# Optimization experiments

Hardware: AMD Instinct MI355X
Metric: run time of the kernel (lower is better)

## Reference

```python
import jax, jax.numpy as jnp
import numpy as np

VQ_NUM = 3
EMB_NUM = 1024
COMMITMENT_WEIGHT = 1.0
# cumprod of [1, emb_num, emb_num] -> per-stage index bases
CUMPROD = [1, EMB_NUM, EMB_NUM * EMB_NUM]


def setup_inputs() -> dict:
    key = jax.random.key(0)
    k0, k1, k2, k3 = jax.random.split(key, 4)
    z = jax.random.normal(k0, (8, 4096, 512), dtype=jnp.float32)
    # linear_in: nn.Linear(in_ch=512, emb_ch=256, bias=False) -> weight [emb_ch, in_ch]
    W_in = jax.random.normal(k1, (VQ_NUM, 256, 512), dtype=jnp.float32) * 0.02
    # linear_out: nn.Linear(emb_ch=256, in_ch=512, bias=False) -> weight [in_ch, emb_ch]
    W_out = jax.random.normal(k2, (VQ_NUM, 512, 256), dtype=jnp.float32) * 0.02
    # one codebook per stage (share_residual_codebooks=False)
    codebooks = jax.random.normal(k3, (VQ_NUM, EMB_NUM, 256), dtype=jnp.float32) * 0.02
    return {"z": z, "W_in": W_in, "W_out": W_out, "codebooks": codebooks}


def reference(z, W_in, W_out, codebooks):
    sg = jax.lax.stop_gradient
    z_q = jnp.zeros_like(z)
    r = z
    loss = jnp.float32(0.0)
    index_sum = jnp.zeros(z.shape[:2], dtype=jnp.int64 if jax.config.jax_enable_x64 else jnp.int32)
    for i in range(VQ_NUM):
        # linear_in
        zi = jnp.einsum('bnc,ec->bne', r, W_in[i])  # [B,N,emb_ch]
        v = codebooks[i]  # [S, emb_ch]
        # squared L2 distance: ||z||^2 + ||v||^2 - 2 z.v
        dist = (jnp.sum(zi * zi, axis=-1, keepdims=True)
                + jnp.sum(v * v, axis=-1)
                - 2.0 * jnp.einsum('bne,se->bns', zi, v))  # [B,N,S]
        idx = jnp.argmin(dist, axis=-1)  # [B,N] int
        zq = v[idx]  # codebook lookup, [B,N,emb_ch]
        loss = loss + (COMMITMENT_WEIGHT * jnp.mean((sg(zq) - zi) ** 2)
                       + jnp.mean((zq - sg(zi)) ** 2))
        # straight-through estimator
        zq_ste = zi + sg(zq - zi)
        # linear_out
        r_q = jnp.einsum('bne,ce->bnc', zq_ste, W_out[i])  # [B,N,in_ch]
        index_sum = index_sum + idx.astype(index_sum.dtype) * CUMPROD[i]
        z_q = z_q + r_q
        r = z - sg(z_q)
    loss = loss / VQ_NUM + jnp.mean((z_q - z) ** 2)
    return z_q, index_sum, loss
```

## Files before the change

### kernel.cpp

```cpp
#include <hip/hip_runtime.h>

#define MTOK 32768
#define CIN  512
#define EMB  256
#define NCODE 1024
#define VQ   3
#define DELTA 2e-3f

typedef short s16x8 __attribute__((ext_vector_type(8)));
typedef float f32x4 __attribute__((ext_vector_type(4)));
typedef unsigned short u16;
typedef unsigned int u32;

static __device__ __forceinline__ u16 f2bf(float x) {
    unsigned int u = __float_as_uint(x);
    u += 0x7FFF + ((u >> 16) & 1);
    return (u16)(u >> 16);
}
static __device__ __forceinline__ float bf2f(u16 h) {
    return __uint_as_float(((unsigned int)h) << 16);
}

__global__ void init_k(double* loss_acc, int* cnt) {
    loss_acc[0] = 0.0;
    loss_acc[1] = 0.0;
    #pragma unroll
    for (int i = 0; i < 8; ++i) cnt[i] = 0;
}

__global__ __launch_bounds__(64) void prep_cb_k(const float* __restrict__ cbs,
                                                double* __restrict__ vnorm64,
                                                float* __restrict__ vnorm32,
                                                u16* __restrict__ cbh,
                                                u16* __restrict__ cbl) {
    int s = blockIdx.x;
    const float* row = cbs + (size_t)s * EMB;
    double acc = 0.0;
    for (int k = threadIdx.x; k < EMB; k += 64) {
        float v = row[k];
        double vd = (double)v; acc += vd * vd;
        u16 h = f2bf(v);
        u16 l = f2bf(v - bf2f(h));
        cbh[(size_t)s * EMB + k] = h;
        cbl[(size_t)s * EMB + k] = l;
    }
    #pragma unroll
    for (int off = 32; off > 0; off >>= 1) acc += __shfl_down(acc, off, 64);
    if (threadIdx.x == 0) { vnorm64[s] = acc; vnorm32[s] = (float)acc; }
}

__global__ __launch_bounds__(256) void prep_w_k(const float* __restrict__ W_in,
                                                u16* __restrict__ wh,
                                                u16* __restrict__ wl) {
    int i = blockIdx.x * 256 + threadIdx.x;
    float v = W_in[i];
    u16 h = f2bf(v);
    wh[i] = h;
    wl[i] = f2bf(v - bf2f(h));
}

__global__ __launch_bounds__(256) void prep_wt_k(const float* __restrict__ W_in,
                                                 float* __restrict__ WinT) {
    int i = blockIdx.x * 256 + threadIdx.x;
    int s = i / (EMB * CIN);
    int rem = i - s * (EMB * CIN);
    int e = rem / CIN;
    int k = rem - e * CIN;
    WinT[(size_t)s * CIN * EMB + (size_t)k * EMB + e] = W_in[i];
}

__global__ __launch_bounds__(256) void prep_T_k(const float* __restrict__ cbs,
                                                const float* __restrict__ Wout,
                                                float* __restrict__ T) {
    const int stage = blockIdx.z;
    const float* A = cbs  + (size_t)stage * NCODE * EMB;
    const float* B = Wout + (size_t)stage * CIN * EMB;
    float* C = T + (size_t)stage * NCODE * CIN;
    __shared__ float As[64][33];
    __shared__ float Bs[64][33];
    const int tid = threadIdx.x;
    const int ty = tid >> 4, tx = tid & 15;
    const int m0 = blockIdx.x * 64;
    const int n0 = blockIdx.y * 64;
    const int lrow = tid >> 5, lcol = tid & 31;
    double acc[4][4];
    #pragma unroll
    for (int i = 0; i < 4; ++i)
        #pragma unroll
        for (int j = 0; j < 4; ++j) acc[i][j] = 0.0;

    for (int k0 = 0; k0 < EMB; k0 += 32) {
        __syncthreads();
        #pragma unroll
        for (int t = 0; t < 8; ++t) {
            int r = lrow + 8 * t;
            As[r][lcol] = A[(size_t)(m0 + r) * EMB + k0 + lcol];
            Bs[r][lcol] = B[(size_t)(n0 + r) * EMB + k0 + lcol];
        }
        __syncthreads();
        #pragma unroll
        for (int k = 0; k < 32; ++k) {
            double a[4], b[4];
            #pragma unroll
            for (int i = 0; i < 4; ++i) a[i] = (double)As[ty * 4 + i][k];
            #pragma unroll
            for (int j = 0; j < 4; ++j) b[j] = (double)Bs[tx * 4 + j][k];
            #pragma unroll
            for (int i = 0; i < 4; ++i)
                #pragma unroll
                for (int j = 0; j < 4; ++j) acc[i][j] += a[i] * b[j];
        }
    }
    #pragma unroll
    for (int i = 0; i < 4; ++i) {
        float4 v = make_float4((float)acc[i][0], (float)acc[i][1],
                               (float)acc[i][2], (float)acc[i][3]);
        *reinterpret_cast<float4*>(&C[(size_t)(m0 + ty * 4 + i) * CIN + n0 + tx * 4]) = v;
    }
}

__global__ __launch_bounds__(256, 2) void fused_k(const float* __restrict__ z,
                                                  const float* __restrict__ zq,
                                                  const u16* __restrict__ wh,
                                                  const u16* __restrict__ wl,
                                                  const u16* __restrict__ cbh,
                                                  const u16* __restrict__ cbl,
                                                  const float* __restrict__ vnorm32,
                                                  u32* __restrict__ zi_hl,
                                                  int* __restrict__ idx,
                                                  int* __restrict__ idx_sum,
                                                  float* __restrict__ mind,
                                                  int* __restrict__ flagged,
                                                  int* __restrict__ cnt,
                                                  int* __restrict__ fullList,
                                                  int* __restrict__ cntF,
                                                  int* __restrict__ cand2,
                                                  double* __restrict__ loss_acc,
                                                  int stage0, int cumprod) {
    __shared__ __align__(16) u16 sbh[2][16][264];
    __shared__ __align__(16) u16 sbl[2][16][264];
    __shared__ double loss_s[16];
    const int tid = threadIdx.x;
    const int w = tid >> 6;
    const int l = tid & 63;
    const int col = l & 15;
    const int g = l >> 4;
    const int mw = blockIdx.x * 64 + w * 16;
    const int sr = tid >> 4, sq = tid & 15;

    {
        s16x8 ah[16], al[16];
        const float* zr = z  + (size_t)(mw + col) * CIN + g * 8;
        const float* qr = zq + (size_t)(mw + col) * CIN + g * 8;
        #pragma unroll
        for (int kc = 0; kc < 16; ++kc) {
            float4 f0 = *reinterpret_cast<const float4*>(zr + kc * 32);
            float4 f1 = *reinterpret_cast<const float4*>(zr + kc * 32 + 4);
            float f[8] = {f0.x, f0.y, f0.z, f0.w, f1.x, f1.y, f1.z, f1.w};
            if (!stage0) {
                float4 q0 = *reinterpret_cast<const float4*>(qr + kc * 32);
                float4 q1 = *reinterpret_cast<const float4*>(qr + kc * 32 + 4);
                f[0] -= q0.x; f[1] -= q0.y; f[2] -= q0.z; f[3] -= q0.w;
                f[4] -= q1.x; f[5] -= q1.y; f[6] -= q1.z; f[7] -= q1.w;
            }
            #pragma unroll
            for (int j = 0; j < 8; ++j) {
                u16 h = f2bf(f[j]);
                u16 lo = f2bf(f[j] - bf2f(h));
                ah[kc][j] = (short)h; al[kc][j] = (short)lo;
            }
        }

        const u16* gwh = wh + (size_t)sr * CIN + sq * 8;
        const u16* gwl = wl + (size_t)sr * CIN + sq * 8;
        uint4 h0, h1, h2, h3, l0, l1, l2, l3;
#define WLOAD(NT) do { const u16* th = gwh + (size_t)(NT) * (16 * CIN);               \
    const u16* tl = gwl + (size_t)(NT) * (16 * CIN);                                  \
    h0 = *(const uint4*)(th);        h1 = *(const uint4*)(th + 128);                  \
    h2 = *(const uint4*)(th + 256);  h3 = *(const uint4*)(th + 384);                  \
    l0 = *(const uint4*)(tl);        l1 = *(const uint4*)(tl + 128);                  \
    l2 = *(const uint4*)(tl + 256);  l3 = *(const uint4*)(tl + 384); } while (0)
#define WWRITE() do {                                                                 \
    *(uint4*)&sbh[0][sr][sq * 8]       = h0;  *(uint4*)&sbh[0][sr][sq * 8 + 128] = h1;\
    *(uint4*)&sbh[1][sr][sq * 8]       = h2;  *(uint4*)&sbh[1][sr][sq * 8 + 128] = h3;\
    *(uint4*)&sbl[0][sr][sq * 8]       = l0;  *(uint4*)&sbl[0][sr][sq * 8 + 128] = l1;\
    *(uint4*)&sbl[1][sr][sq * 8]       = l2;  *(uint4*)&sbl[1][sr][sq * 8 + 128] = l3;\
    } while (0)
        WLOAD(0);

        double zn = 0.0;
        for (int nt = 0; nt < 16; ++nt) {
            __syncthreads();
            WWRITE();
            __syncthreads();
            if (nt + 1 < 16) WLOAD(nt + 1);
            f32x4 a0 = {0.f, 0.f, 0.f, 0.f};
            f32x4 a1 = {0.f, 0.f, 0.f, 0.f};
            f32x4 a2 = {0.f, 0.f, 0.f, 0.f};
            #pragma unroll
            for (int kc = 0; kc < 16; ++kc) {
                const int p = kc >> 3;
                const int ko = (kc & 7) * 32 + g * 8;
                s16x8 Bh = *(const s16x8*)&sbh[p][col][ko];
                s16x8 Bl = *(const s16x8*)&sbl[p][col][ko];
                a0 = __builtin_amdgcn_mfma_f32_16x16x32_bf16(ah[kc], Bh, a0, 0, 0, 0);
                a1 = __builtin_amdgcn_mfma_f32_16x16x32_bf16(al[kc], Bh, a1, 0, 0, 0);
                a2 = __builtin_amdgcn_mfma_f32_16x16x32_bf16(ah[kc], Bl, a2, 0, 0, 0);
            }
            #pragma unroll
            for (int r = 0; r < 4; ++r) {
                float v = a0[r] + a1[r] + a2[r];
                u16 h = f2bf(v);
                u16 lo = f2bf(v - bf2f(h));
                zi_hl[(size_t)(mw + g * 4 + r) * EMB + nt * 16 + col] =
                    (u32)h | ((u32)lo << 16);
                zn += (double)v * (double)v;
            }
        }
#undef WLOAD
#undef WWRITE
        #pragma unroll
        for (int off = 32; off > 0; off >>= 1) zn += __shfl_down(zn, off, 64);
        if (l == 0) atomicAdd(loss_acc, zn);
    }
    __syncthreads();

    s16x8 ah[8], al[8];
    {
        const u32* zr = zi_hl + (size_t)(mw + col) * EMB + g * 8;
        #pragma unroll
        for (int kc = 0; kc < 8; ++kc) {
            uint4 u0 = *reinterpret_cast<const uint4*>(zr + kc * 32);
            uint4 u1 = *reinterpret_cast<const uint4*>(zr + kc * 32 + 4);
            u32 u[8] = {u0.x, u0.y, u0.z, u0.w, u1.x, u1.y, u1.z, u1.w};
            #pragma unroll
            for (int j = 0; j < 8; ++j) {
                ah[kc][j] = (short)(u[j] & 0xffffu);
                al[kc][j] = (short)(u[j] >> 16);
            }
        }
    }

    float b1[4] = {1e30f, 1e30f, 1e30f, 1e30f};
    float b2[4] = {1e30f, 1e30f, 1e30f, 1e30f};
    float b3[4] = {1e30f, 1e30f, 1e30f, 1e30f};
    int   i1[4] = {0, 0, 0, 0};
    int   i2[4] = {0, 0, 0, 0};

    const u16* gh = cbh + (size_t)sr * EMB + sq * 8;
    const u16* gl = cbl + (size_t)sr * EMB + sq * 8;
    uint4 h0, h1, l0, l1;
#define PLOAD(CT) do { const u16* th = gh + (size_t)(CT) * (16 * EMB);                \
    const u16* tl = gl + (size_t)(CT) * (16 * EMB);                                   \
    h0 = *(const uint4*)(th);  h1 = *(const uint4*)(th + 128);                        \
    l0 = *(const uint4*)(tl);  l1 = *(const uint4*)(tl + 128); } while (0)
#define PWRITE(P) do {                                                                \
    *(uint4*)&sbh[P][sr][sq * 8] = h0;  *(uint4*)&sbh[P][sr][sq * 8 + 128] = h1;      \
    *(uint4*)&sbl[P][sr][sq * 8] = l0;  *(uint4*)&sbl[P][sr][sq * 8 + 128] = l1;      \
    } while (0)
    PLOAD(0); PWRITE(0); PLOAD(1);

    for (int ct = 0; ct < 64; ++ct) {
        __syncthreads();
        const int p = ct & 1;
        if (ct + 1 < 64) PWRITE((ct + 1) & 1);
        if (ct + 2 < 64) PLOAD(ct + 2);
        const float vn = vnorm32[ct * 16 + col];
        f32x4 a0 = {0.f, 0.f, 0.f, 0.f};
        f32x4 a1 = {0.f, 0.f, 0.f, 0.f};
        f32x4 a2 = {0.f, 0.f, 0.f, 0.f};
        #pragma unroll
        for (int kc = 0; kc < 8; ++kc) {
            s16x8 Bh = *(const s16x8*)&sbh[p][col][g * 8 + kc * 32];
            s16x8 Bl = *(const s16x8*)&sbl[p][col][g * 8 + kc * 32];
            a0 = __builtin_amdgcn_mfma_f32_16x16x32_bf16(ah[kc], Bh, a0, 0, 0, 0);
            a1 = __builtin_amdgcn_mfma_f32_16x16x32_bf16(al[kc], Bh, a1, 0, 0, 0);
            a2 = __builtin_amdgcn_mfma_f32_16x16x32_bf16(ah[kc], Bl, a2, 0, 0, 0);
        }
        #pragma unroll
        for (int r = 0; r < 4; ++r) {
            float sc = vn - 2.f * (a0[r] + a1[r] + a2[r]);
            int c = ct * 16 + col;
            if (sc < b1[r]) { b3[r] = b2[r]; b2[r] = b1[r]; i2[r] = i1[r]; b1[r] = sc; i1[r] = c; }
            else if (sc < b2[r]) { b3[r] = b2[r]; b2[r] = sc; i2[r] = c; }
            else b3[r] = fminf(b3[r], sc);
        }
    }
#undef PLOAD
#undef PWRITE

    #pragma unroll
    for (int off = 1; off < 16; off <<= 1) {
        #pragma unroll
        for (int r = 0; r < 4; ++r) {
            float c1 = __shfl_xor(b1[r], off, 64);
            int   j1 = __shfl_xor(i1[r], off, 64);
            float c2 = __shfl_xor(b2[r], off, 64);
            int   j2 = __shfl_xor(i2[r], off, 64);
            float c3 = __shfl_xor(b3[r], off, 64);
            float nb1, nb2, nb3; int ni1, ni2;
            if (c1 < b1[r] || (c1 == b1[r] && j1 < i1[r])) {
                nb1 = c1; ni1 = j1;
                if (b1[r] < c2 || (b1[r] == c2 && i1[r] < j2)) {
                    nb2 = b1[r]; ni2 = i1[r]; nb3 = fminf(b2[r], c2);
                } else {
                    nb2 = c2; ni2 = j2; nb3 = fminf(b1[r], c3);
                }
            } else {
                nb1 = b1[r]; ni1 = i1[r];
                if (c1 < b2[r] || (c1 == b2[r] && j1 < i2[r])) {
                    nb2 = c1; ni2 = j1; nb3 = fminf(b2[r], c2);
                } else {
                    nb2 = b2[r]; ni2 = i2[r]; nb3 = fminf(c1, b3[r]);
                }
            }
            b1[r] = nb1; b2[r] = nb2; b3[r] = nb3; i1[r] = ni1; i2[r] = ni2;
        }
    }
    if (col == 0) {
        double lsum = 0.0;
        #pragma unroll
        for (int r = 0; r < 4; ++r) {
            int m = mw + g * 4 + r;
            idx[m] = i1[r];
            if (stage0) idx_sum[m] = i1[r];
            else        idx_sum[m] += i1[r] * cumprod;
            mind[m] = b1[r];
            lsum += (double)b1[r];
            if (b2[r] - b1[r] < DELTA) {
                if (b3[r] - b1[r] < DELTA) {
                    int slot = atomicAdd(cntF, 1);
                    fullList[slot] = m;
                } else {
                    int slot = atomicAdd(cnt, 1);
                    flagged[slot] = m;
                    cand2[m] = i2[r];
                }
            }
        }
        loss_s[w * 4 + g] = lsum;
    }
    __syncthreads();
    if (tid == 0) {
        double s = 0.0;
        #pragma unroll
        for (int q = 0; q < 16; ++q) s += loss_s[q];
        atomicAdd(loss_acc, s);
    }
}

__global__ __launch_bounds__(256) void rescan_pair_k(const float* __restrict__ z,
                                                     const float* __restrict__ zqv,
                                                     const float* __restrict__ WinT,
                                                     const float* __restrict__ cb,
                                                     const double* __restrict__ vnorm64,
                                                     const int* __restrict__ flagged,
                                                     const int* __restrict__ cnt,
                                                     const int* __restrict__ cand2,
                                                     int* __restrict__ idx,
                                                     int* __restrict__ idx_sum,
                                                     float* __restrict__ mind,
                                                     double* __restrict__ loss_acc,
                                                     int cumprod, int stage0) {
    __shared__ double r64[8][CIN];
    __shared__ int mArr[8], cAArr[8], cBArr[8];
    double* zi_l = &r64[0][0];
    const int tid = threadIdx.x;
    const int w = tid >> 6, l = tid & 63;
    const int n = *cnt;

    for (int jb = blockIdx.x; jb * 8 < n; jb += gridDim.x) {
        const int nt = min(8, n - jb * 8);
        __syncthreads();
        if (tid < nt) {
            int m = flagged[jb * 8 + tid];
            mArr[tid] = m;
            cAArr[tid] = idx[m]; cBArr[tid] = cand2[m];
        }
        __syncthreads();
        for (int t = 0; t < nt; ++t) {
            const int m = mArr[t];
            #pragma unroll
            for (int h = 0; h < 2; ++h) {
                int k = tid + h * 256;
                float rv = z[(size_t)m * CIN + k];
                if (!stage0) rv -= zqv[(size_t)m * CIN + k];
                r64[t][k] = (double)rv;
            }
        }
        __syncthreads();
        double acc[8] = {0, 0, 0, 0, 0, 0, 0, 0};
        #pragma unroll 4
        for (int k = 0; k < CIN; ++k) {
            double wv = (double)WinT[(size_t)k * EMB + tid];
            #pragma unroll
            for (int t = 0; t < 8; ++t) acc[t] += r64[t][k] * wv;
        }
        __syncthreads();
        #pragma unroll
        for (int t = 0; t < 8; ++t) zi_l[t * 256 + tid] = acc[t];
        __syncthreads();

        for (int t = w; t < nt; t += 4) {
            const int cA = cAArr[t], cB = cBArr[t], m = mArr[t];
            const double* zt = zi_l + t * 256;
            float4 vA = *(const float4*)(cb + (size_t)cA * EMB + 4 * l);
            float4 vB = *(const float4*)(cb + (size_t)cB * EMB + 4 * l);
            double z0 = zt[4 * l], z1 = zt[4 * l + 1];
            double z2 = zt[4 * l + 2], z3 = zt[4 * l + 3];
            double sA = z0 * (double)vA.x + z1 * (double)vA.y
                      + z2 * (double)vA.z + z3 * (double)vA.w;
            double sB = z0 * (double)vB.x + z1 * (double)vB.y
                      + z2 * (double)vB.z + z3 * (double)vB.w;
            #pragma unroll
            for (int off = 1; off < 64; off <<= 1) {
                sA += __shfl_xor(sA, off, 64);
                sB += __shfl_xor(sB, off, 64);
            }
            if (l == 0) {
                double dA = vnorm64[cA] - 2.0 * sA;
                double dB = vnorm64[cB] - 2.0 * sB;
                int bi; double best;
                if (dB < dA || (dB == dA && cB < cA)) { bi = cB; best = dB; }
                else                                   { bi = cA; best = dA; }
                int oldI = idx[m];
                if (bi != oldI) { idx[m] = bi; idx_sum[m] += (bi - oldI) * cumprod; }
                atomicAdd(loss_acc, best - (double)mind[m]);
                mind[m] = (float)best;
            }
        }
    }
}

__global__ __launch_bounds__(256) void fullscan_k(const float* __restrict__ z,
                                                  const float* __restrict__ zqv,
                                                  const float* __restrict__ WinT,
                                                  const float* __restrict__ cb,
                                                  const double* __restrict__ vnorm64,
                                                  const int* __restrict__ fullList,
                                                  const int* __restrict__ cntF,
                                                  int* __restrict__ idx,
                                                  int* __restrict__ idx_sum,
                                                  float* __restrict__ mind,
                                                  double* __restrict__ loss_acc,
                                                  int cumprod, int stage0) {
    __shared__ double r64[CIN];
    __shared__ double zi64[EMB];
    __shared__ double sred[256];
    __shared__ int ired[256];
    const int tid = threadIdx.x;
    const int n = *cntF;

    for (int j = blockIdx.x; j < n; j += gridDim.x) {
        const int m = fullList[j];
        __syncthreads();
        #pragma unroll
        for (int h = 0; h < 2; ++h) {
            int k = tid + h * 256;
            float rv = z[(size_t)m * CIN + k];
            if (!stage0) rv -= zqv[(size_t)m * CIN + k];
            r64[k] = (double)rv;
        }
        __syncthreads();
        {
            double acc = 0.0;
            #pragma unroll 8
            for (int k = 0; k < CIN; ++k)
                acc += r64[k] * (double)WinT[(size_t)k * EMB + tid];
            zi64[tid] = acc;
        }
        __syncthreads();
        double best = 1e300; int bi = 0;
        #pragma unroll
        for (int q = 0; q < 4; ++q) {
            const int c = q * 256 + tid;
            const float* row = cb + (size_t)c * EMB;
            double s0 = 0, s1 = 0, s2 = 0, s3 = 0;
            #pragma unroll 4
            for (int e = 0; e < EMB; e += 4) {
                float4 v = *(const float4*)(row + e);
                s0 += zi64[e]     * (double)v.x;
                s1 += zi64[e + 1] * (double)v.y;
                s2 += zi64[e + 2] * (double)v.z;
                s3 += zi64[e + 3] * (double)v.w;
            }
            double sc = vnorm64[c] - 2.0 * ((s0 + s1) + (s2 + s3));
            if (sc < best) { best = sc; bi = c; }
        }
        sred[tid] = best; ired[tid] = bi;
        __syncthreads();
        for (int off = 128; off > 0; off >>= 1) {
            if (tid < off) {
                double ob = sred[tid + off]; int oi = ired[tid + off];
                if (ob < sred[tid] || (ob == sred[tid] && oi < ired[tid])) {
                    sred[tid] = ob; ired[tid] = oi;
                }
            }
            __syncthreads();
        }
        if (tid == 0) {
            int oldI = idx[m], bi2 = ired[0];
            double best2 = sred[0];
            if (bi2 != oldI) { idx[m] = bi2; idx_sum[m] += (bi2 - oldI) * cumprod; }
            atomicAdd(loss_acc, best2 - (double)mind[m]);
            mind[m] = (float)best2;
        }
    }
}

__global__ __launch_bounds__(256) void gather_k(const float* __restrict__ T,
                                                const int* __restrict__ idx,
                                                const float* __restrict__ z,
                                                float* __restrict__ zq,
                                                int stage0, int last,
                                                double* __restrict__ loss_acc) {
    __shared__ double red[256];
    int m = blockIdx.x * 16 + (threadIdx.x >> 4);
    int q = threadIdx.x & 15;
    const float* src = T + (size_t)idx[m] * CIN;
    float* dst = zq + (size_t)m * CIN;
    double s = 0.0;
    #pragma unroll
    for (int it = 0; it < 8; ++it) {
        int off = it * 64 + q * 4;
        float4 t = *reinterpret_cast<const float4*>(src + off);
        if (!stage0) {
            float4 o = *reinterpret_cast<const float4*>(dst + off);
            t.x += o.x; t.y += o.y; t.z += o.z; t.w += o.w;
        }
        *reinterpret_cast<float4*>(dst + off) = t;
        if (last) {
            float4 zv = *reinterpret_cast<const float4*>(z + (size_t)m * CIN + off);
            double d0 = (double)zv.x - (double)t.x;
            double d1 = (double)zv.y - (double)t.y;
            double d2 = (double)zv.z - (double)t.z;
            double d3 = (double)zv.w - (double)t.w;
            s += d0 * d0 + d1 * d1 + d2 * d2 + d3 * d3;
        }
    }
    if (last) {
        red[threadIdx.x] = s;
        __syncthreads();
        for (int off = 128; off > 0; off >>= 1) {
            if (threadIdx.x < off) red[threadIdx.x] += red[threadIdx.x + off];
            __syncthreads();
        }
        if (threadIdx.x == 0) atomicAdd(loss_acc + 1, red[0]);
    }
}

__global__ void final_k(const int* __restrict__ idx_sum,
                        const double* __restrict__ loss_acc,
                        float* __restrict__ out) {
    int i = blockIdx.x * blockDim.x + threadIdx.x;
    if (i < MTOK) out[MTOK * CIN + i] = (float)idx_sum[i];
    if (i == 0) {
        double loss = 2.0 * loss_acc[0] / (3.0 * (double)MTOK * (double)EMB)
                    + loss_acc[1] / ((double)MTOK * (double)CIN);
        out[MTOK * CIN + MTOK] = (float)loss;
    }
}

extern "C" void kernel_launch(void* const* d_in, const int* in_sizes, int n_in,
                              void* d_out, int out_size, void* d_ws, size_t ws_size,
                              hipStream_t stream) {
    const float* z     = (const float*)d_in[0];
    const float* W_in  = (const float*)d_in[1];
    const float* W_out = (const float*)d_in[2];
    const float* cbs   = (const float*)d_in[3];
    float* out = (float*)d_out;
    char* ws = (char*)d_ws;

    double* vnorm64  = (double*)ws;
    double* loss_acc = (double*)(ws + 24576);
    int*    cnt      = (int*)(ws + 24592);
    float*  vnorm32  = (float*)(ws + 24624);
    u16*    cbh      = (u16*)(ws + 36912);
    u16*    cbl      = (u16*)(ws + 1609776);
    u16*    wh       = (u16*)(ws + 3182640);
    u16*    wl       = (u16*)(ws + 3969072);
    float*  WinT     = (float*)(ws + 4755504);
    float*  T        = (float*)(ws + 6328368);
    u32*    zi_hl    = (u32*)(ws + 12619824);
    char*   p        = ws + 46174256;
    int*    idx      = (int*)p;
    int*    idx_sum  = (int*)(p + 131072);
    int*    flagged  = (int*)(p + 262144);
    float*  mind     = (float*)(p + 393216);
    int*    cand2    = (int*)(p + 524288);
    int*    fullList = (int*)(p + 655360);

    float* zq = out;

    init_k<<<dim3(1), dim3(1), 0, stream>>>(loss_acc, cnt);
    prep_cb_k<<<dim3(VQ * NCODE), dim3(64), 0, stream>>>(cbs, vnorm64, vnorm32, cbh, cbl);
    prep_w_k<<<dim3(VQ * EMB * CIN / 256), dim3(256), 0, stream>>>(W_in, wh, wl);
    prep_wt_k<<<dim3(VQ * EMB * CIN / 256), dim3(256), 0, stream>>>(W_in, WinT);
    prep_T_k<<<dim3(NCODE / 64, CIN / 64, VQ), dim3(256), 0, stream>>>(cbs, W_out, T);

    const int cumprod[VQ] = {1, 1024, 1024 * 1024};
    for (int i = 0; i < VQ; ++i) {
        const float* cb = cbs + (size_t)i * NCODE * EMB;
        fused_k<<<dim3(MTOK / 64), dim3(256), 0, stream>>>(
            z, zq, wh + (size_t)i * EMB * CIN, wl + (size_t)i * EMB * CIN,
            cbh + (size_t)i * NCODE * EMB, cbl + (size_t)i * NCODE * EMB,
            vnorm32 + i * NCODE, zi_hl, idx, idx_sum, mind, flagged, cnt + i,
            fullList, cnt + 3 + i, cand2, loss_acc, i == 0 ? 1 : 0, cumprod[i]);
        rescan_pair_k<<<dim3(512), dim3(256), 0, stream>>>(
            z, zq, WinT + (size_t)i * EMB * CIN, cb, vnorm64 + i * NCODE,
            flagged, cnt + i, cand2, idx, idx_sum, mind, loss_acc, cumprod[i],
            i == 0 ? 1 : 0);
        fullscan_k<<<dim3(256), dim3(256), 0, stream>>>(
            z, zq, WinT + (size_t)i * EMB * CIN, cb, vnorm64 + i * NCODE,
            fullList, cnt + 3 + i, idx, idx_sum, mind, loss_acc, cumprod[i],
            i == 0 ? 1 : 0);
        gather_k<<<dim3(MTOK / 16), dim3(256), 0, stream>>>(
            T + (size_t)i * NCODE * CIN, idx, z, zq, i == 0 ? 1 : 0,
            i == VQ - 1 ? 1 : 0, loss_acc);
    }
    final_k<<<dim3(MTOK / 256), dim3(256), 0, stream>>>(idx_sum, loss_acc, out);
}
```

Measured before the change: 876.2 us.

## Keep projected zi in LDS instead of global scratch, swizzle tiles

The fused kernel now holds the projected hi/lo bf16 zi rows in a 64 KB shared buffer instead of writing them to a global workspace and reading them back. Weight and codebook tiles move to single-buffered, XOR-swizzled LDS tiles to avoid bank conflicts, with the W_in tiles split into K halves. The block loss reduction becomes a wave shuffle plus per-wave atomic. The trade-off is much higher LDS use, which may reduce occupancy, and an extra barrier per tile from losing double buffering.

```diff
diff --git a/kernel.cpp b/kernel.cpp
--- a/kernel.cpp
+++ b/kernel.cpp
@@ -126,7 +126,6 @@
                                                   const u16* __restrict__ cbh,
                                                   const u16* __restrict__ cbl,
                                                   const float* __restrict__ vnorm32,
-                                                  u32* __restrict__ zi_hl,
                                                   int* __restrict__ idx,
                                                   int* __restrict__ idx_sum,
                                                   float* __restrict__ mind,
@@ -137,9 +136,9 @@
                                                   int* __restrict__ cand2,
                                                   double* __restrict__ loss_acc,
                                                   int stage0, int cumprod) {
-    __shared__ __align__(16) u16 sbh[2][16][264];
-    __shared__ __align__(16) u16 sbl[2][16][264];
-    __shared__ double loss_s[16];
+    __shared__ __align__(16) u32 zi_lds[64][256];
+    __shared__ __align__(16) u16 sbh[16][256];
+    __shared__ __align__(16) u16 sbl[16][256];
     const int tid = threadIdx.x;
     const int w = tid >> 6;
     const int l = tid & 63;
@@ -147,6 +146,7 @@
     const int g = l >> 4;
     const int mw = blockIdx.x * 64 + w * 16;
     const int sr = tid >> 4, sq = tid & 15;
+    const int swz_w = (sq ^ (sr & 7)) << 3;
 
     {
         s16x8 ah[16], al[16];
@@ -171,67 +171,66 @@
             }
         }
 
-        const u16* gwh = wh + (size_t)sr * CIN + sq * 8;
-        const u16* gwl = wl + (size_t)sr * CIN + sq * 8;
-        uint4 h0, h1, h2, h3, l0, l1, l2, l3;
-#define WLOAD(NT) do { const u16* th = gwh + (size_t)(NT) * (16 * CIN);               \
-    const u16* tl = gwl + (size_t)(NT) * (16 * CIN);                                  \
-    h0 = *(const uint4*)(th);        h1 = *(const uint4*)(th + 128);                  \
-    h2 = *(const uint4*)(th + 256);  h3 = *(const uint4*)(th + 384);                  \
-    l0 = *(const uint4*)(tl);        l1 = *(const uint4*)(tl + 128);                  \
-    l2 = *(const uint4*)(tl + 256);  l3 = *(const uint4*)(tl + 384); } while (0)
-#define WWRITE() do {                                                                 \
-    *(uint4*)&sbh[0][sr][sq * 8]       = h0;  *(uint4*)&sbh[0][sr][sq * 8 + 128] = h1;\
-    *(uint4*)&sbh[1][sr][sq * 8]       = h2;  *(uint4*)&sbh[1][sr][sq * 8 + 128] = h3;\
-    *(uint4*)&sbl[0][sr][sq * 8]       = l0;  *(uint4*)&sbl[0][sr][sq * 8 + 128] = l1;\
-    *(uint4*)&sbl[1][sr][sq * 8]       = l2;  *(uint4*)&sbl[1][sr][sq * 8 + 128] = l3;\
-    } while (0)
+        uint4 h0, h1, l0, l1;
+#define WLOAD(S) do { int nt_ = (S) >> 1, kh_ = (S) & 1;                               \
+    const u16* th = wh + (size_t)(nt_ * 16 + sr) * CIN + kh_ * 256 + sq * 8;           \
+    const u16* tl = wl + (size_t)(nt_ * 16 + sr) * CIN + kh_ * 256 + sq * 8;           \
+    h0 = *(const uint4*)(th);  h1 = *(const uint4*)(th + 128);                         \
+    l0 = *(const uint4*)(tl);  l1 = *(const uint4*)(tl + 128); } while (0)
+#define SWRITE() do {                                                                  \
+    *(uint4*)&sbh[sr][swz_w] = h0;  *(uint4*)&sbh[sr][swz_w + 128] = h1;               \
+    *(uint4*)&sbl[sr][swz_w] = l0;  *(uint4*)&sbl[sr][swz_w + 128] = l1; } while (0)
         WLOAD(0);
 
         double zn = 0.0;
         for (int nt = 0; nt < 16; ++nt) {
-            __syncthreads();
-            WWRITE();
-            __syncthreads();
-            if (nt + 1 < 16) WLOAD(nt + 1);
             f32x4 a0 = {0.f, 0.f, 0.f, 0.f};
             f32x4 a1 = {0.f, 0.f, 0.f, 0.f};
             f32x4 a2 = {0.f, 0.f, 0.f, 0.f};
             #pragma unroll
-            for (int kc = 0; kc < 16; ++kc) {
-                const int p = kc >> 3;
-                const int ko = (kc & 7) * 32 + g * 8;
-                s16x8 Bh = *(const s16x8*)&sbh[p][col][ko];
-                s16x8 Bl = *(const s16x8*)&sbl[p][col][ko];
-                a0 = __builtin_amdgcn_mfma_f32_16x16x32_bf16(ah[kc], Bh, a0, 0, 0, 0);
-                a1 = __builtin_amdgcn_mfma_f32_16x16x32_bf16(al[kc], Bh, a1, 0, 0, 0);
-                a2 = __builtin_amdgcn_mfma_f32_16x16x32_bf16(ah[kc], Bl, a2, 0, 0, 0);
+            for (int kh = 0; kh < 2; ++kh) {
+                const int S = nt * 2 + kh;
+                __syncthreads();
+                SWRITE();
+                __syncthreads();
+                if (S + 1 < 32) WLOAD(S + 1);
+                #pragma unroll
+                for (int kc = 0; kc < 8; ++kc) {
+                    const int off = (((g + 4 * kc) ^ (col & 7)) << 3);
+                    s16x8 Bh = *(const s16x8*)&sbh[col][off];
+                    s16x8 Bl = *(const s16x8*)&sbl[col][off];
+                    const int ka = kh * 8 + kc;
+                    a0 = __builtin_amdgcn_mfma_f32_16x16x32_bf16(ah[ka], Bh, a0, 0, 0, 0);
+                    a1 = __builtin_amdgcn_mfma_f32_16x16x32_bf16(al[ka], Bh, a1, 0, 0, 0);
+                    a2 = __builtin_amdgcn_mfma_f32_16x16x32_bf16(ah[ka], Bl, a2, 0, 0, 0);
+                }
             }
             #pragma unroll
             for (int r = 0; r < 4; ++r) {
                 float v = a0[r] + a1[r] + a2[r];
                 u16 h = f2bf(v);
                 u16 lo = f2bf(v - bf2f(h));
-                zi_hl[(size_t)(mw + g * 4 + r) * EMB + nt * 16 + col] =
-                    (u32)h | ((u32)lo << 16);
+                const int trow = w * 16 + g * 4 + r;
+                const int coff = (((nt * 4 + (col >> 2)) ^ (trow & 7)) << 2) + (col & 3);
+                zi_lds[trow][coff] = (u32)h | ((u32)lo << 16);
                 zn += (double)v * (double)v;
             }
         }
 #undef WLOAD
-#undef WWRITE
+#undef SWRITE
         #pragma unroll
         for (int off = 32; off > 0; off >>= 1) zn += __shfl_down(zn, off, 64);
         if (l == 0) atomicAdd(loss_acc, zn);
     }
-    __syncthreads();
 
     s16x8 ah[8], al[8];
     {
-        const u32* zr = zi_hl + (size_t)(mw + col) * EMB + g * 8;
+        const int t = w * 16 + col;
         #pragma unroll
         for (int kc = 0; kc < 8; ++kc) {
-            uint4 u0 = *reinterpret_cast<const uint4*>(zr + kc * 32);
-            uint4 u1 = *reinterpret_cast<const uint4*>(zr + kc * 32 + 4);
+            const int ck0 = g * 2 + kc * 8;
+            uint4 u0 = *(const uint4*)&zi_lds[t][((ck0 ^ (t & 7)) << 2)];
+            uint4 u1 = *(const uint4*)&zi_lds[t][(((ck0 + 1) ^ (t & 7)) << 2)];
             u32 u[8] = {u0.x, u0.y, u0.z, u0.w, u1.x, u1.y, u1.z, u1.w};
             #pragma unroll
             for (int j = 0; j < 8; ++j) {
@@ -247,32 +246,31 @@
     int   i1[4] = {0, 0, 0, 0};
     int   i2[4] = {0, 0, 0, 0};
 
-    const u16* gh = cbh + (size_t)sr * EMB + sq * 8;
-    const u16* gl = cbl + (size_t)sr * EMB + sq * 8;
     uint4 h0, h1, l0, l1;
-#define PLOAD(CT) do { const u16* th = gh + (size_t)(CT) * (16 * EMB);                \
-    const u16* tl = gl + (size_t)(CT) * (16 * EMB);                                   \
-    h0 = *(const uint4*)(th);  h1 = *(const uint4*)(th + 128);                        \
+#define PLOAD(CT) do {                                                                 \
+    const u16* th = cbh + (size_t)((CT) * 16 + sr) * EMB + sq * 8;                     \
+    const u16* tl = cbl + (size_t)((CT) * 16 + sr) * EMB + sq * 8;                     \
+    h0 = *(const uint4*)(th);  h1 = *(const uint4*)(th + 128);                         \
     l0 = *(const uint4*)(tl);  l1 = *(const uint4*)(tl + 128); } while (0)
-#define PWRITE(P) do {                                                                \
-    *(uint4*)&sbh[P][sr][sq * 8] = h0;  *(uint4*)&sbh[P][sr][sq * 8 + 128] = h1;      \
-    *(uint4*)&sbl[P][sr][sq * 8] = l0;  *(uint4*)&sbl[P][sr][sq * 8 + 128] = l1;      \
-    } while (0)
-    PLOAD(0); PWRITE(0); PLOAD(1);
+#define SWRITE() do {                                                                  \
+    *(uint4*)&sbh[sr][swz_w] = h0;  *(uint4*)&sbh[sr][swz_w + 128] = h1;               \
+    *(uint4*)&sbl[sr][swz_w] = l0;  *(uint4*)&sbl[sr][swz_w + 128] = l1; } while (0)
+    PLOAD(0);
 
     for (int ct = 0; ct < 64; ++ct) {
         __syncthreads();
-        const int p = ct & 1;
-        if (ct + 1 < 64) PWRITE((ct + 1) & 1);
-        if (ct + 2 < 64) PLOAD(ct + 2);
+        SWRITE();
+        __syncthreads();
+        if (ct + 1 < 64) PLOAD(ct + 1);
         const float vn = vnorm32[ct * 16 + col];
         f32x4 a0 = {0.f, 0.f, 0.f, 0.f};
         f32x4 a1 = {0.f, 0.f, 0.f, 0.f};
         f32x4 a2 = {0.f, 0.f, 0.f, 0.f};
         #pragma unroll
         for (int kc = 0; kc < 8; ++kc) {
-            s16x8 Bh = *(const s16x8*)&sbh[p][col][g * 8 + kc * 32];
-            s16x8 Bl = *(const s16x8*)&sbl[p][col][g * 8 + kc * 32];
+            const int off = (((g + 4 * kc) ^ (col & 7)) << 3);
+            s16x8 Bh = *(const s16x8*)&sbh[col][off];
+            s16x8 Bl = *(const s16x8*)&sbl[col][off];
             a0 = __builtin_amdgcn_mfma_f32_16x16x32_bf16(ah[kc], Bh, a0, 0, 0, 0);
             a1 = __builtin_amdgcn_mfma_f32_16x16x32_bf16(al[kc], Bh, a1, 0, 0, 0);
             a2 = __builtin_amdgcn_mfma_f32_16x16x32_bf16(ah[kc], Bl, a2, 0, 0, 0);
@@ -287,7 +285,7 @@
         }
     }
 #undef PLOAD
-#undef PWRITE
+#undef SWRITE
 
     #pragma unroll
     for (int off = 1; off < 16; off <<= 1) {
@@ -317,8 +315,9 @@
             b1[r] = nb1; b2[r] = nb2; b3[r] = nb3; i1[r] = ni1; i2[r] = ni2;
         }
     }
+
+    double lsum = 0.0;
     if (col == 0) {
-        double lsum = 0.0;
         #pragma unroll
         for (int r = 0; r < 4; ++r) {
             int m = mw + g * 4 + r;
@@ -338,15 +337,10 @@
                 }
             }
         }
-        loss_s[w * 4 + g] = lsum;
-    }
-    __syncthreads();
-    if (tid == 0) {
-        double s = 0.0;
-        #pragma unroll
-        for (int q = 0; q < 16; ++q) s += loss_s[q];
-        atomicAdd(loss_acc, s);
-    }
+    }
+    #pragma unroll
+    for (int off = 32; off > 0; off >>= 1) lsum += __shfl_down(lsum, off, 64);
+    if (l == 0) atomicAdd(loss_acc, lsum);
 }
 
 __global__ __launch_bounds__(256) void rescan_pair_k(const float* __restrict__ z,
@@ -581,8 +575,7 @@
     u16*    wl       = (u16*)(ws + 3969072);
     float*  WinT     = (float*)(ws + 4755504);
     float*  T        = (float*)(ws + 6328368);
-    u32*    zi_hl    = (u32*)(ws + 12619824);
-    char*   p        = ws + 46174256;
+    char*   p        = ws + 12619824;
     int*    idx      = (int*)p;
     int*    idx_sum  = (int*)(p + 131072);
     int*    flagged  = (int*)(p + 262144);
@@ -604,7 +597,7 @@
         fused_k<<<dim3(MTOK / 64), dim3(256), 0, stream>>>(
             z, zq, wh + (size_t)i * EMB * CIN, wl + (size_t)i * EMB * CIN,
             cbh + (size_t)i * NCODE * EMB, cbl + (size_t)i * NCODE * EMB,
-            vnorm32 + i * NCODE, zi_hl, idx, idx_sum, mind, flagged, cnt + i,
+            vnorm32 + i * NCODE, idx, idx_sum, mind, flagged, cnt + i,
             fullList, cnt + 3 + i, cand2, loss_acc, i == 0 ? 1 : 0, cumprod[i]);
         rescan_pair_k<<<dim3(512), dim3(256), 0, stream>>>(
             z, zq, WinT + (size_t)i * EMB * CIN, cb, vnorm64 + i * NCODE,
```

New measurement: 924.6 us. +5.5%, slower.

## Double-buffer linear_in weight tiles, add MFMA priority hints, cheaper bf16 split

Applied to the files above, without the earlier changes.

The linear_in GEMM loop previously staged a full 16x512 weight tile in shared memory with two barriers per tile. It now splits each tile into two K-halves that are double-buffered, so the next half is written and loaded while the current half computes, needing one barrier per step. s_setprio hints are placed around the MFMA loops in both the projection and distance phases. The hi/lo bf16 split now uses truncation instead of round-to-nearest. That changes the rounding of the hi part, but the residual lo term still carries most of the lost precision.

```diff
diff --git a/kernel.cpp b/kernel.cpp
--- a/kernel.cpp
+++ b/kernel.cpp
@@ -19,6 +19,12 @@
 }
 static __device__ __forceinline__ float bf2f(u16 h) {
     return __uint_as_float(((unsigned int)h) << 16);
+}
+static __device__ __forceinline__ void split2(float v, u16& h, u16& lo) {
+    u32 u = __float_as_uint(v);
+    h = (u16)(u >> 16);
+    float d = v - __uint_as_float(u & 0xFFFF0000u);
+    lo = (u16)(__float_as_uint(d) >> 16);
 }
 
 __global__ void init_k(double* loss_acc, int* cnt) {
@@ -165,53 +171,50 @@
             }
             #pragma unroll
             for (int j = 0; j < 8; ++j) {
-                u16 h = f2bf(f[j]);
-                u16 lo = f2bf(f[j] - bf2f(h));
+                u16 h, lo; split2(f[j], h, lo);
                 ah[kc][j] = (short)h; al[kc][j] = (short)lo;
             }
         }
 
-        const u16* gwh = wh + (size_t)sr * CIN + sq * 8;
-        const u16* gwl = wl + (size_t)sr * CIN + sq * 8;
-        uint4 h0, h1, h2, h3, l0, l1, l2, l3;
-#define WLOAD(NT) do { const u16* th = gwh + (size_t)(NT) * (16 * CIN);               \
-    const u16* tl = gwl + (size_t)(NT) * (16 * CIN);                                  \
-    h0 = *(const uint4*)(th);        h1 = *(const uint4*)(th + 128);                  \
-    h2 = *(const uint4*)(th + 256);  h3 = *(const uint4*)(th + 384);                  \
-    l0 = *(const uint4*)(tl);        l1 = *(const uint4*)(tl + 128);                  \
-    l2 = *(const uint4*)(tl + 256);  l3 = *(const uint4*)(tl + 384); } while (0)
-#define WWRITE() do {                                                                 \
-    *(uint4*)&sbh[0][sr][sq * 8]       = h0;  *(uint4*)&sbh[0][sr][sq * 8 + 128] = h1;\
-    *(uint4*)&sbh[1][sr][sq * 8]       = h2;  *(uint4*)&sbh[1][sr][sq * 8 + 128] = h3;\
-    *(uint4*)&sbl[0][sr][sq * 8]       = l0;  *(uint4*)&sbl[0][sr][sq * 8 + 128] = l1;\
-    *(uint4*)&sbl[1][sr][sq * 8]       = l2;  *(uint4*)&sbl[1][sr][sq * 8 + 128] = l3;\
+        uint4 h0, h1, l0, l1;
+#define WLOAD(S) do { int nt_ = (S) >> 1, kh_ = (S) & 1;                               \
+    const u16* th = wh + (size_t)(nt_ * 16 + sr) * CIN + kh_ * 256 + sq * 8;           \
+    const u16* tl = wl + (size_t)(nt_ * 16 + sr) * CIN + kh_ * 256 + sq * 8;           \
+    h0 = *(const uint4*)(th);  h1 = *(const uint4*)(th + 128);                         \
+    l0 = *(const uint4*)(tl);  l1 = *(const uint4*)(tl + 128); } while (0)
+#define WWRITE(P) do {                                                                 \
+    *(uint4*)&sbh[P][sr][sq * 8] = h0;  *(uint4*)&sbh[P][sr][sq * 8 + 128] = h1;       \
+    *(uint4*)&sbl[P][sr][sq * 8] = l0;  *(uint4*)&sbl[P][sr][sq * 8 + 128] = l1;       \
     } while (0)
-        WLOAD(0);
+        WLOAD(0); WWRITE(0); WLOAD(1);
 
         double zn = 0.0;
         for (int nt = 0; nt < 16; ++nt) {
-            __syncthreads();
-            WWRITE();
-            __syncthreads();
-            if (nt + 1 < 16) WLOAD(nt + 1);
             f32x4 a0 = {0.f, 0.f, 0.f, 0.f};
             f32x4 a1 = {0.f, 0.f, 0.f, 0.f};
             f32x4 a2 = {0.f, 0.f, 0.f, 0.f};
             #pragma unroll
-            for (int kc = 0; kc < 16; ++kc) {
-                const int p = kc >> 3;
-                const int ko = (kc & 7) * 32 + g * 8;
-                s16x8 Bh = *(const s16x8*)&sbh[p][col][ko];
-                s16x8 Bl = *(const s16x8*)&sbl[p][col][ko];
-                a0 = __builtin_amdgcn_mfma_f32_16x16x32_bf16(ah[kc], Bh, a0, 0, 0, 0);
-                a1 = __builtin_amdgcn_mfma_f32_16x16x32_bf16(al[kc], Bh, a1, 0, 0, 0);
-                a2 = __builtin_amdgcn_mfma_f32_16x16x32_bf16(ah[kc], Bl, a2, 0, 0, 0);
+            for (int kh = 0; kh < 2; ++kh) {
+                const int S = nt * 2 + kh;
+                __syncthreads();
+                if (S + 1 < 32) WWRITE((S + 1) & 1);
+                if (S + 2 < 32) WLOAD(S + 2);
+                __builtin_amdgcn_s_setprio(1);
+                #pragma unroll
+                for (int kc = 0; kc < 8; ++kc) {
+                    s16x8 Bh = *(const s16x8*)&sbh[kh][col][g * 8 + kc * 32];
+                    s16x8 Bl = *(const s16x8*)&sbl[kh][col][g * 8 + kc * 32];
+                    const int ka = kh * 8 + kc;
+                    a0 = __builtin_amdgcn_mfma_f32_16x16x32_bf16(ah[ka], Bh, a0, 0, 0, 0);
+                    a1 = __builtin_amdgcn_mfma_f32_16x16x32_bf16(al[ka], Bh, a1, 0, 0, 0);
+                    a2 = __builtin_amdgcn_mfma_f32_16x16x32_bf16(ah[ka], Bl, a2, 0, 0, 0);
+                }
+                __builtin_amdgcn_s_setprio(0);
             }
             #pragma unroll
             for (int r = 0; r < 4; ++r) {
                 float v = a0[r] + a1[r] + a2[r];
-                u16 h = f2bf(v);
-                u16 lo = f2bf(v - bf2f(h));
+                u16 h, lo; split2(v, h, lo);
                 zi_hl[(size_t)(mw + g * 4 + r) * EMB + nt * 16 + col] =
                     (u32)h | ((u32)lo << 16);
                 zn += (double)v * (double)v;
@@ -247,16 +250,15 @@
     int   i1[4] = {0, 0, 0, 0};
     int   i2[4] = {0, 0, 0, 0};
 
-    const u16* gh = cbh + (size_t)sr * EMB + sq * 8;
-    const u16* gl = cbl + (size_t)sr * EMB + sq * 8;
     uint4 h0, h1, l0, l1;
-#define PLOAD(CT) do { const u16* th = gh + (size_t)(CT) * (16 * EMB);                \
-    const u16* tl = gl + (size_t)(CT) * (16 * EMB);                                   \
-    h0 = *(const uint4*)(th);  h1 = *(const uint4*)(th + 128);                        \
+#define PLOAD(CT) do {                                                                 \
+    const u16* th = cbh + (size_t)((CT) * 16 + sr) * EMB + sq * 8;                     \
+    const u16* tl = cbl + (size_t)((CT) * 16 + sr) * EMB + sq * 8;                     \
+    h0 = *(const uint4*)(th);  h1 = *(const uint4*)(th + 128);                         \
     l0 = *(const uint4*)(tl);  l1 = *(const uint4*)(tl + 128); } while (0)
-#define PWRITE(P) do {                                                                \
-    *(uint4*)&sbh[P][sr][sq * 8] = h0;  *(uint4*)&sbh[P][sr][sq * 8 + 128] = h1;      \
-    *(uint4*)&sbl[P][sr][sq * 8] = l0;  *(uint4*)&sbl[P][sr][sq * 8 + 128] = l1;      \
+#define PWRITE(P) do {                                                                 \
+    *(uint4*)&sbh[P][sr][sq * 8] = h0;  *(uint4*)&sbh[P][sr][sq * 8 + 128] = h1;       \
+    *(uint4*)&sbl[P][sr][sq * 8] = l0;  *(uint4*)&sbl[P][sr][sq * 8 + 128] = l1;       \
     } while (0)
     PLOAD(0); PWRITE(0); PLOAD(1);
 
@@ -269,6 +271,7 @@
         f32x4 a0 = {0.f, 0.f, 0.f, 0.f};
         f32x4 a1 = {0.f, 0.f, 0.f, 0.f};
         f32x4 a2 = {0.f, 0.f, 0.f, 0.f};
+        __builtin_amdgcn_s_setprio(1);
         #pragma unroll
         for (int kc = 0; kc < 8; ++kc) {
             s16x8 Bh = *(const s16x8*)&sbh[p][col][g * 8 + kc * 32];
@@ -277,6 +280,7 @@
             a1 = __builtin_amdgcn_mfma_f32_16x16x32_bf16(al[kc], Bh, a1, 0, 0, 0);
             a2 = __builtin_amdgcn_mfma_f32_16x16x32_bf16(ah[kc], Bl, a2, 0, 0, 0);
         }
+        __builtin_amdgcn_s_setprio(0);
         #pragma unroll
         for (int r = 0; r < 4; ++r) {
             float sc = vn - 2.f * (a0[r] + a1[r] + a2[r]);
```

Measured after the change: 844.0 us. -3.7%, faster.
